# Performance work log

Measured on AMD Instinct MI355X. Metric: run time of the kernel, lower is better.

## Reference

```python
import jax, jax.numpy as jnp
import numpy as np

B, S, HN, TN = 8, 32, 64, 512
HID, EMB, VOCAB = 512, 512, 10000


def setup_inputs():
    key = jax.random.key(0)
    k = jax.random.split(key, 14)
    w = lambda kk, shape: jax.random.normal(kk, shape, jnp.float32) * 0.02
    return {
        "dec_out": jax.random.normal(k[0], (B, S, HID), jnp.float32),
        "history": jax.random.normal(k[1], (B, HID), jnp.float32),
        "head": jax.random.randint(k[2], (B, HN), 0, VOCAB),
        "tail": jax.random.randint(k[3], (B, TN), 0, VOCAB),
        "adj_mask": jax.random.randint(k[4], (B, HN, TN), 0, 2).astype(bool),
        "dup_mask": jax.random.randint(k[5], (B, S, TN), 0, 2).astype(bool),
        "emb_table": w(k[6], (VOCAB, EMB)),
        "W_tq": w(k[7], (2 * HID + EMB, HID)),
        "b_tq": jnp.zeros((HID,), jnp.float32),
        "W_tk": w(k[8], (EMB, HID)),
        "b_tk": jnp.zeros((HID,), jnp.float32),
        "W_tout": w(k[9], (2 * HID, HID)),
        "W_hq": w(k[10], (2 * HID, HID)),
        "b_hq": jnp.zeros((HID,), jnp.float32),
        "W_hk": w(k[11], (HID, HID)),
        "b_hk": jnp.zeros((HID,), jnp.float32),
    }


def reference(dec_out, history, head, tail, adj_mask, dup_mask, emb_table,
              W_tq, b_tq, W_tk, b_tk, W_tout, W_hq, b_hq, W_hk, b_hk):
    head_emb = emb_table[head]  # (B, HN, EMB)
    tail_emb = emb_table[tail]  # (B, TN, EMB)

    # --- tail attention query: Linear(cat([dec_out, history, head_emb])) + ELU.
    # Same math as the torch broadcast-concat, computed as a sum of three
    # partial matmuls to avoid materializing the (B,S,HN,2*hid+emb) concat.
    Wd, Wh, We = W_tq[:HID], W_tq[HID:2 * HID], W_tq[2 * HID:]
    tq = jax.nn.elu((dec_out @ Wd)[:, :, None, :]
                    + (history @ Wh)[:, None, None, :]
                    + (head_emb @ We)[:, None, :, :]
                    + b_tq)                       # (B, S, HN, HID)
    tq = tq.reshape(B, S * HN, HID)
    tk = jax.nn.elu(tail_emb @ W_tk + b_tk)       # (B, TN, HID)  (dropout=eval)

    # combined logical mask: allowed = adjacency AND not-duplicate
    mask = (adj_mask[:, None, :, :] & ~dup_mask[:, :, None, :]).reshape(B, S * HN, TN)

    # GlobalAttention (dot): score -> mask -> softmax -> context -> tanh(linear_out([c;q]))
    scores = jnp.einsum('bqh,bth->bqt', tq, tk)   # (B, S*HN, TN)
    tail_attn = jax.nn.softmax(jnp.where(mask, scores, -jnp.inf), axis=-1)
    ctx = jnp.einsum('bqt,bth->bqh', tail_attn, tk)
    graph_hid = jnp.tanh(ctx @ W_tout[:HID] + tq @ W_tout[HID:])
    graph_hid = graph_hid.reshape(B * S, HN, HID)
    tail_attn = tail_attn.reshape(B * S, HN, TN)

    # --- head attention (one-step), length-masked over HN
    hq = jax.nn.elu(dec_out @ W_hq[:HID] + (history @ W_hq[HID:])[:, None, :] + b_hq)
    hq = hq.reshape(B * S, HID)
    hk = jax.nn.elu(jnp.einsum('nkh,hd->nkd', graph_hid, W_hk) + b_hk)
    lengths = jnp.repeat(jnp.sum(head != 0, axis=-1), S)          # (B*S,)
    hscores = jnp.einsum('nh,nkh->nk', hq, hk)                    # (B*S, HN)
    lmask = jnp.arange(HN)[None, :] < lengths[:, None]
    head_attn = jax.nn.softmax(jnp.where(lmask, hscores, -jnp.inf), axis=-1)
    # (head-attention context output is discarded by the original module)

    prob = jnp.einsum('nk,nkt->nt', head_attn, tail_attn).reshape(B, S, TN)
    return jnp.log(prob + 1e-20)
```

## Files before the change

### kernel.cpp

```cpp
#include <hip/hip_runtime.h>
#include <math.h>

#define BB 8
#define SS 32
#define HN 64
#define TN 512
#define HID 512

typedef __attribute__((ext_vector_type(8))) short short8;
typedef __attribute__((ext_vector_type(4))) float f32x4;

__device__ __forceinline__ float eluf(float x) { return x > 0.f ? x : (expf(x) - 1.f); }

__device__ __forceinline__ short f2bs(float f) {
    union { float f; unsigned int u; } v; v.f = f;
    unsigned int r = v.u + 0x7fffu + ((v.u >> 16) & 1u);
    return (short)(r >> 16);
}
__device__ __forceinline__ float b2f(short s) {
    union { unsigned int u; float f; } v;
    v.u = ((unsigned int)(unsigned short)s) << 16;
    return v.f;
}

__device__ __forceinline__ void gld16(const void* g, void* l) {
    __builtin_amdgcn_global_load_lds(
        (const __attribute__((address_space(1))) void*)g,
        (__attribute__((address_space(3))) void*)l, 16, 0, 0);
}

template <int ACT, int OUTB>
__device__ __forceinline__ void gcore(
    const short* __restrict__ A, const short* __restrict__ B,
    const float* __restrict__ bias, void* __restrict__ Cv,
    int ldc, int K, int m0, int n0, int cm0, short* Ls)
{
    short* Al = Ls;
    short* Bl = Ls + 8192;
    const int tid  = threadIdx.x;
    const int lane = tid & 63;
    const int w    = tid >> 6;
    const int wr   = w >> 1, wc = w & 1;
    const int l16  = lane & 15, quad = lane >> 4;

    const int srow = w * 16 + (lane >> 2);
    const int scol = (lane & 3) * 8;

    f32x4 acc[4][4];
#pragma unroll
    for (int i = 0; i < 4; ++i)
#pragma unroll
        for (int j = 0; j < 4; ++j) { acc[i][j][0]=0.f; acc[i][j][1]=0.f; acc[i][j][2]=0.f; acc[i][j][3]=0.f; }

    short* lA = Al + w * 512;
    short* lB = Bl + w * 512;
    const long rstep = (long)64 * K;

    const short* Ag = A + (long)(m0 + srow) * K + scol;
    const short* Bg = B + (long)(n0 + srow) * K + scol;
    for (int kt = 0; kt < K; kt += 64) {
        __syncthreads();
        gld16(Ag + kt, lA);
        gld16(Ag + kt + rstep, lA + 2048);
        gld16(Ag + kt + 32, lA + 4096);
        gld16(Ag + kt + 32 + rstep, lA + 4096 + 2048);
        gld16(Bg + kt, lB);
        gld16(Bg + kt + rstep, lB + 2048);
        gld16(Bg + kt + 32, lB + 4096);
        gld16(Bg + kt + 32 + rstep, lB + 4096 + 2048);
        __syncthreads();
#pragma unroll
        for (int h = 0; h < 2; ++h) {
            short8 af[4], bf4[4];
#pragma unroll
            for (int mi = 0; mi < 4; ++mi)
                af[mi] = *(const short8*)(Al + h * 4096 + (wr * 64 + mi * 16 + l16) * 32 + quad * 8);
#pragma unroll
            for (int ni = 0; ni < 4; ++ni)
                bf4[ni] = *(const short8*)(Bl + h * 4096 + (wc * 64 + ni * 16 + l16) * 32 + quad * 8);
#pragma unroll
            for (int mi = 0; mi < 4; ++mi)
#pragma unroll
                for (int ni = 0; ni < 4; ++ni)
                    acc[mi][ni] = __builtin_amdgcn_mfma_f32_16x16x32_bf16(af[mi], bf4[ni], acc[mi][ni], 0, 0, 0);
        }
    }

    __syncthreads();

    float bv[4];
#pragma unroll
    for (int ni = 0; ni < 4; ++ni)
        bv[ni] = bias ? bias[n0 + wc * 64 + ni * 16 + l16] : 0.f;

    if (OUTB == 1) {
        short* eb = Ls + w * 1152;
        const int er = lane >> 2;
        const int ec = (lane & 3) * 16;
#pragma unroll
        for (int mi = 0; mi < 4; ++mi) {
#pragma unroll
            for (int ni = 0; ni < 4; ++ni)
#pragma unroll
                for (int r = 0; r < 4; ++r) {
                    float x = acc[mi][ni][r] + bv[ni];
                    if (ACT == 1) x = eluf(x);
                    eb[(quad * 4 + r) * 72 + ni * 16 + l16] = f2bs(x);
                }
            __builtin_amdgcn_sched_barrier(0);
            short8 v0 = *(const short8*)&eb[er * 72 + ec];
            short8 v1 = *(const short8*)&eb[er * 72 + ec + 8];
            long cb = (long)(cm0 + wr * 64 + mi * 16 + er) * ldc + n0 + wc * 64 + ec;
            *(short8*)((short*)Cv + cb)     = v0;
            *(short8*)((short*)Cv + cb + 8) = v1;
            __builtin_amdgcn_sched_barrier(0);
        }
    } else {
#pragma unroll
        for (int mi = 0; mi < 4; ++mi)
#pragma unroll
            for (int ni = 0; ni < 4; ++ni) {
                int gc = n0 + wc * 64 + ni * 16 + l16;
#pragma unroll
                for (int r = 0; r < 4; ++r) {
                    float x = acc[mi][ni][r] + bv[ni];
                    if (ACT == 1) x = eluf(x);
                    ((float*)Cv)[(long)(cm0 + wr * 64 + mi * 16 + quad * 4 + r) * ldc + gc] = x;
                }
            }
    }
}

template <int ACT, int OUTB, int DUAL>
__device__ __forceinline__ void gcoreB(
    const short* __restrict__ A, const short* __restrict__ B,
    const short* __restrict__ A2, const short* __restrict__ B2,
    const float* __restrict__ bias, void* __restrict__ Cv,
    int ldc, int K, int m0, int n0, int cm0, short* Ls,
    const float* __restrict__ hq, float* __restrict__ hsp)
{
    short* Al = Ls;
    short* Bl = Ls + 16384;
    const int tid  = threadIdx.x;
    const int lane = tid & 63;
    const int w    = tid >> 6;
    const int wr   = w >> 1, wc = w & 1;
    const int l16  = lane & 15, quad = lane >> 4;

    const int srow = w * 16 + (lane >> 2);
    const int scol = (lane & 3) * 8;

    f32x4 acc[4][4];
#pragma unroll
    for (int i = 0; i < 4; ++i)
#pragma unroll
        for (int j = 0; j < 4; ++j) { acc[i][j][0]=0.f; acc[i][j][1]=0.f; acc[i][j][2]=0.f; acc[i][j][3]=0.f; }

    short* lA = Al + w * 512;
    short* lB = Bl + w * 512;
    const long rstep = (long)64 * K;

    for (int rep = 0; rep <= DUAL; ++rep) {
        const short* Ag = (rep ? A2 : A) + (long)(m0 + srow) * K + scol;
        const short* Bg = (rep ? B2 : B) + (long)(n0 + srow) * K + scol;
        for (int kt = 0; kt < K; kt += 128) {
            __syncthreads();
#pragma unroll
            for (int h = 0; h < 4; ++h) {
                gld16(Ag + kt + h * 32,         lA + h * 4096);
                gld16(Ag + kt + h * 32 + rstep, lA + h * 4096 + 2048);
                gld16(Bg + kt + h * 32,         lB + h * 4096);
                gld16(Bg + kt + h * 32 + rstep, lB + h * 4096 + 2048);
            }
            __syncthreads();
#pragma unroll
            for (int h = 0; h < 4; ++h) {
                short8 af[4], bf4[4];
#pragma unroll
                for (int mi = 0; mi < 4; ++mi)
                    af[mi] = *(const short8*)(Al + h * 4096 + (wr * 64 + mi * 16 + l16) * 32 + quad * 8);
#pragma unroll
                for (int ni = 0; ni < 4; ++ni)
                    bf4[ni] = *(const short8*)(Bl + h * 4096 + (wc * 64 + ni * 16 + l16) * 32 + quad * 8);
#pragma unroll
                for (int mi = 0; mi < 4; ++mi)
#pragma unroll
                    for (int ni = 0; ni < 4; ++ni)
                        acc[mi][ni] = __builtin_amdgcn_mfma_f32_16x16x32_bf16(af[mi], bf4[ni], acc[mi][ni], 0, 0, 0);
            }
        }
    }

    __syncthreads();

    float bv[4];
#pragma unroll
    for (int ni = 0; ni < 4; ++ni)
        bv[ni] = bias ? bias[n0 + wc * 64 + ni * 16 + l16] : 0.f;

    if (OUTB == 1) {
        short* eb = Ls + w * 1152;
        const int er = lane >> 2;
        const int ec = (lane & 3) * 16;
#pragma unroll
        for (int mi = 0; mi < 4; ++mi) {
#pragma unroll
            for (int ni = 0; ni < 4; ++ni)
#pragma unroll
                for (int r = 0; r < 4; ++r) {
                    float x = acc[mi][ni][r] + bv[ni];
                    if (ACT == 1) x = eluf(x);
                    else if (ACT == 2) x = tanhf(x);
                    eb[(quad * 4 + r) * 72 + ni * 16 + l16] = f2bs(x);
                }
            __builtin_amdgcn_sched_barrier(0);
            short8 v0 = *(const short8*)&eb[er * 72 + ec];
            short8 v1 = *(const short8*)&eb[er * 72 + ec + 8];
            long cb = (long)(cm0 + wr * 64 + mi * 16 + er) * ldc + n0 + wc * 64 + ec;
            *(short8*)((short*)Cv + cb)     = v0;
            *(short8*)((short*)Cv + cb + 8) = v1;
            __builtin_amdgcn_sched_barrier(0);
        }
    } else if (OUTB == 2) {
        const int n_w = (cm0 + wr * 64) >> 6;
        float hqv[4];
#pragma unroll
        for (int ni = 0; ni < 4; ++ni)
            hqv[ni] = hq[(long)n_w * 512 + n0 + wc * 64 + ni * 16 + l16];
        float* red = (float*)Ls;
#pragma unroll
        for (int mi = 0; mi < 4; ++mi)
#pragma unroll
            for (int r = 0; r < 4; ++r) {
                float p = 0.f;
#pragma unroll
                for (int ni = 0; ni < 4; ++ni) {
                    float x = acc[mi][ni][r] + bv[ni];
                    if (ACT == 1) x = eluf(x);
                    p += x * hqv[ni];
                }
                p += __shfl_xor(p, 1);
                p += __shfl_xor(p, 2);
                p += __shfl_xor(p, 4);
                p += __shfl_xor(p, 8);
                if (l16 == 0) red[w * 64 + mi * 16 + quad * 4 + r] = p;
            }
        __syncthreads();
        if (tid < 128) {
            int wr2 = tid >> 6, rw = tid & 63;
            float v = red[(wr2 * 2 + 0) * 64 + rw] + red[(wr2 * 2 + 1) * 64 + rw];
            hsp[(long)(n0 >> 7) * 16384 + cm0 + tid] = v;
        }
    }
}

template <int ACT, int OUTB, int DUAL, int NYL2>
__global__ __launch_bounds__(256) void mgemm_sw(
    const short* __restrict__ A, long sAz,
    const short* __restrict__ B, long sBz,
    const short* __restrict__ A2, long sA2z,
    const short* __restrict__ B2,
    const float* __restrict__ bias,
    void* __restrict__ Cv, long sCz, int ldc, int K)
{
    __shared__ short Ls[32768];
    const int bid = blockIdx.x;
    const int g = (bid & 7) + 8 * (bid >> 5);
    const int x = (bid >> 3) & 3;
    const int y = g & ((1 << NYL2) - 1);
    const int z = g >> NYL2;
    void* C = (void*)((short*)Cv + (long)z * sCz);
    const short* A2z = DUAL ? (A2 + (long)z * sA2z) : nullptr;
    gcoreB<ACT, OUTB, DUAL>(A + (long)z * sAz, B + (long)z * sBz, A2z, B2, bias, C,
                            ldc, K, y * 128, x * 128, y * 128, Ls, nullptr, nullptr);
}

__global__ __launch_bounds__(256) void mgemm_hs(
    const short* __restrict__ A, const short* __restrict__ B,
    const float* __restrict__ bias, const float* __restrict__ hq, float* __restrict__ hsp)
{
    __shared__ short Ls[32768];
    const int bid = blockIdx.x;
    const int y = (bid & 7) + 8 * (bid >> 5);
    const int x = (bid >> 3) & 3;
    gcoreB<1, 2, 0>(A, B, nullptr, nullptr, bias, nullptr, 512, 512,
                    y * 128, x * 128, y * 128, Ls, hq, hsp);
}

__global__ __launch_bounds__(256) void mgemm_multi(
    const short* __restrict__ decb, const short* __restrict__ WTall, float* __restrict__ qall,
    const short* __restrict__ embAll, const short* __restrict__ WTe, float* __restrict__ qe,
    const short* __restrict__ WTk, const float* __restrict__ b_tk, short* __restrict__ tkb)
{
    __shared__ short Ls[16384];
    int id = blockIdx.x;
    if (id < 48) {
        int y = id >> 4, x = id & 15;
        gcore<0, 0>(decb, WTall, nullptr, qall, 2048, 512, y * 128, x * 128, y * 128, Ls);
    } else if (id < 64) {
        int id2 = id - 48, y = id2 >> 2, x = id2 & 3;
        gcore<0, 0>(embAll, WTe, nullptr, qe, 512, 512, y * 128, x * 128, y * 128, Ls);
    } else {
        int id3 = id - 64, y = id3 >> 2, x = id3 & 3;
        gcore<1, 1>(embAll, WTk, b_tk, tkb, 512, 512, 512 + y * 128, x * 128, y * 128, Ls);
    }
}

struct WTDesc { const float* src[9]; short* dst[9]; };

__global__ __launch_bounds__(256) void prep(
    const float* __restrict__ dec_out, const float* __restrict__ history,
    short* __restrict__ decb,
    const float* __restrict__ emb, const int* __restrict__ head, const int* __restrict__ tail,
    short* __restrict__ embAll, WTDesc wd)
{
    __shared__ float t[32][33];
    const int id = blockIdx.x, tid = threadIdx.x;
    if (id < 132) {
        int i = (id * 256 + tid) * 4;
        float4 v = (i < 131072) ? *(const float4*)(dec_out + i)
                                : *(const float4*)(history + (i - 131072));
        short4 o;
        o.x = f2bs(v.x); o.y = f2bs(v.y); o.z = f2bs(v.z); o.w = f2bs(v.w);
        *(short4*)(decb + i) = o;
    } else if (id < 132 + 2304) {
        int r = (id - 132) * 2 + (tid >> 7);
        int c4 = (tid & 127) * 4;
        int idx = (r < 512) ? head[r] : tail[r - 512];
        float4 v = *(const float4*)(emb + (long)idx * 512 + c4);
        short4 o;
        o.x = f2bs(v.x); o.y = f2bs(v.y); o.z = f2bs(v.z); o.w = f2bs(v.w);
        *(short4*)(embAll + (long)r * 512 + c4) = o;
    } else {
        int q = id - 2436;
        int z = q >> 8, xy = q & 255;
        int x = xy & 15, y = xy >> 4;
        const float* src = wd.src[z];
        short* dst = wd.dst[z];
        int k0 = y * 32, n0 = x * 32;
        int tx = tid & 31, ty = tid >> 5;
#pragma unroll
        for (int i = 0; i < 32; i += 8)
            t[ty + i][tx] = src[(long)(k0 + ty + i) * 512 + n0 + tx];
        __syncthreads();
#pragma unroll
        for (int i = 0; i < 32; i += 8)
            dst[(long)(n0 + ty + i) * 512 + k0 + tx] = f2bs(t[tx][ty + i]);
    }
}

__global__ __launch_bounds__(256) void l3_kernel(
    const float* __restrict__ qall, const float* __restrict__ qe,
    const float* __restrict__ b_tq, short* __restrict__ tqb,
    const short* __restrict__ WTo1, const short* __restrict__ tkb, short* __restrict__ tkWTb,
    const float* __restrict__ b_hq, float* __restrict__ hqf)
{
    __shared__ short Ls[16384];
    if (blockIdx.x < 8192) {
        long gid = (long)blockIdx.x * 256 + threadIdx.x;
        int r = (int)(gid >> 7), j0 = ((int)gid & 127) * 4;
        int b = r >> 11, rem = r & 2047, s = rem >> 6, h = rem & 63;
        float4 d = *(const float4*)(qall + (long)(b * 32 + s) * 2048 + j0);
        float4 q = *(const float4*)(qall + (long)(256 + b) * 2048 + 1024 + j0);
        float4 e = *(const float4*)(qe + (long)(b * 64 + h) * 512 + j0);
        float4 bb = *(const float4*)(b_tq + j0);
        short4 o;
        o.x = f2bs(eluf(d.x + q.x + e.x + bb.x));
        o.y = f2bs(eluf(d.y + q.y + e.y + bb.y));
        o.z = f2bs(eluf(d.z + q.z + e.z + bb.z));
        o.w = f2bs(eluf(d.w + q.w + e.w + bb.w));
        *(short4*)(tqb + (long)r * 512 + j0) = o;
    } else if (blockIdx.x < 8320) {
        int id2 = blockIdx.x - 8192;
        int z = id2 >> 4, r = id2 & 15;
        int x = r & 3, y = r >> 2;
        gcore<0, 1>(WTo1, tkb + (long)z * 262144, nullptr,
                    tkWTb + (long)z * 262144, 512, 512, y * 128, x * 128, y * 128, Ls);
    } else {
        long gid = (long)(blockIdx.x - 8320) * 256 + threadIdx.x;
        int n = (int)(gid >> 7), j0 = ((int)gid & 127) * 4;
        int b = n >> 5;
        float4 d = *(const float4*)(qall + (long)n * 2048 + 512 + j0);
        float4 h2 = *(const float4*)(qall + (long)(256 + b) * 2048 + 1536 + j0);
        float4 bb = *(const float4*)(b_hq + j0);
        float4 o;
        o.x = eluf(d.x + h2.x + bb.x);
        o.y = eluf(d.y + h2.y + bb.y);
        o.z = eluf(d.z + h2.z + bb.z);
        o.w = eluf(d.w + h2.w + bb.w);
        *(float4*)(hqf + (long)n * 512 + j0) = o;
    }
}

__global__ __launch_bounds__(256) void sm_kernel(
    const short* __restrict__ sc, const int* __restrict__ adj, const int* __restrict__ dup,
    short* __restrict__ Pb)
{
    int w = threadIdx.x >> 6, lane = threadIdx.x & 63;
    long r = (long)blockIdx.x * 4 + w;
    int b = (int)(r >> 11), rem = (int)(r & 2047), s = rem >> 6, h = rem & 63;
    const short* row = sc + r * 512 + lane * 8;
    const int* adjr = adj + ((long)(b * 64 + h)) * 512 + lane * 8;
    const int* dupr = dup + ((long)(b * 32 + s)) * 512 + lane * 8;
    short8 v8 = *(const short8*)row;
    int4 a0 = *(const int4*)adjr, a1 = *(const int4*)(adjr + 4);
    int4 d0 = *(const int4*)dupr, d1 = *(const int4*)(dupr + 4);
    int am[8] = {a0.x, a0.y, a0.z, a0.w, a1.x, a1.y, a1.z, a1.w};
    int dm[8] = {d0.x, d0.y, d0.z, d0.w, d1.x, d1.y, d1.z, d1.w};
    float v[8];
    float m = -INFINITY;
#pragma unroll
    for (int i = 0; i < 8; ++i) {
        v[i] = (am[i] && !dm[i]) ? b2f(v8[i]) : -INFINITY;
        m = fmaxf(m, v[i]);
    }
#pragma unroll
    for (int d = 32; d >= 1; d >>= 1) m = fmaxf(m, __shfl_xor(m, d));
    float sum = 0.f;
#pragma unroll
    for (int i = 0; i < 8; ++i) {
        float e = (m == -INFINITY) ? 0.f : expf(v[i] - m);
        v[i] = e; sum += e;
    }
#pragma unroll
    for (int d = 32; d >= 1; d >>= 1) sum += __shfl_xor(sum, d);
    float inv = sum > 0.f ? 1.f / sum : 0.f;
    short8 o;
#pragma unroll
    for (int i = 0; i < 8; ++i) o[i] = f2bs(v[i] * inv);
    *(short8*)(Pb + r * 512 + lane * 8) = o;
}

__global__ __launch_bounds__(256) void fused_head(
    const float* __restrict__ hsp, const int* __restrict__ head,
    const short* __restrict__ ta, float* __restrict__ out)
{
    int n = blockIdx.x, b = n >> 5;
    int tid = threadIdx.x;
    __shared__ float hal[64];
    __shared__ float part[4][512];

    if (tid < 64) {
        float sv_raw = hsp[n * 64 + tid] + hsp[16384 + n * 64 + tid]
                     + hsp[2 * 16384 + n * 64 + tid] + hsp[3 * 16384 + n * 64 + tid];
        int hv = head[b * 64 + tid];
        unsigned long long ball = __ballot(hv != 0);
        int len = __popcll(ball);
        float sv = (tid < len) ? sv_raw : -INFINITY;
        float m = sv;
#pragma unroll
        for (int d = 32; d >= 1; d >>= 1) m = fmaxf(m, __shfl_xor(m, d));
        float e = expf(sv - m);
        float sum = e;
#pragma unroll
        for (int d = 32; d >= 1; d >>= 1) sum += __shfl_xor(sum, d);
        hal[tid] = e / sum;
    }
    __syncthreads();

    {
        int w = tid >> 6, lane = tid & 63;
        const short* tab = ta + (long)n * 64 * 512 + (long)(w * 16) * 512 + lane * 8;
        float acc[8] = {};
#pragma unroll
        for (int k = 0; k < 16; ++k) {
            float a = hal[w * 16 + k];
            short8 tv = *(const short8*)(tab + (long)k * 512);
#pragma unroll
            for (int u = 0; u < 8; ++u) acc[u] += a * b2f(tv[u]);
        }
        float4* pp = (float4*)&part[w][lane * 8];
        pp[0] = make_float4(acc[0], acc[1], acc[2], acc[3]);
        pp[1] = make_float4(acc[4], acc[5], acc[6], acc[7]);
    }
    __syncthreads();

    for (int t = tid; t < 512; t += 256) {
        float a = part[0][t] + part[1][t] + part[2][t] + part[3][t];
        out[(long)n * 512 + t] = logf(a + 1e-20f);
    }
}

extern "C" void kernel_launch(void* const* d_in, const int* in_sizes, int n_in,
                              void* d_out, int out_size, void* d_ws, size_t ws_size,
                              hipStream_t stream)
{
    const float* dec_out = (const float*)d_in[0];
    const float* history = (const float*)d_in[1];
    const int*   head    = (const int*)d_in[2];
    const int*   tail    = (const int*)d_in[3];
    const int*   adj     = (const int*)d_in[4];
    const int*   dup     = (const int*)d_in[5];
    const float* emb     = (const float*)d_in[6];
    const float* W_tq    = (const float*)d_in[7];
    const float* b_tq    = (const float*)d_in[8];
    const float* W_tk    = (const float*)d_in[9];
    const float* b_tk    = (const float*)d_in[10];
    const float* W_tout  = (const float*)d_in[11];
    const float* W_hq    = (const float*)d_in[12];
    const float* b_hq    = (const float*)d_in[13];
    const float* W_hk    = (const float*)d_in[14];
    const float* b_hk    = (const float*)d_in[15];
    float* out = (float*)d_out;

    char* ws = (char*)d_ws;
    auto alloc = [&](size_t bytes) -> void* {
        char* p = ws;
        ws += (bytes + 255) & ~(size_t)255;
        return (void*)p;
    };
    short* decb   = (short*)alloc((size_t)384 * 512 * 2);
    short* embAll = (short*)alloc((size_t)4608 * 512 * 2);
    short* WT     = (short*)alloc((size_t)9 * 512 * 512 * 2);
    float* qall   = (float*)alloc((size_t)384 * 2048 * 4);
    float* qe     = (float*)alloc((size_t)512 * 512 * 4);
    float* hqf    = (float*)alloc((size_t)256 * 512 * 4);
    float* hsp    = (float*)alloc((size_t)4 * 16384 * 4);
    short* tkb    = (short*)alloc((size_t)4096 * 512 * 2);
    short* tkWTb  = (short*)alloc((size_t)4096 * 512 * 2);
    short* tqb    = (short*)alloc((size_t)16384 * 512 * 2);
    short* scb    = (short*)alloc((size_t)16384 * 512 * 2);
    short* Pb     = (short*)alloc((size_t)16384 * 512 * 2);
    short* ghb = scb;

    WTDesc wd;
    wd.src[0] = W_tq;               wd.dst[0] = WT;
    wd.src[1] = W_hq;               wd.dst[1] = WT + (size_t)1 * 262144;
    wd.src[2] = W_tq + 512 * 512;   wd.dst[2] = WT + (size_t)2 * 262144;
    wd.src[3] = W_hq + 512 * 512;   wd.dst[3] = WT + (size_t)3 * 262144;
    wd.src[4] = W_tq + 1024 * 512;  wd.dst[4] = WT + (size_t)4 * 262144;
    wd.src[5] = W_tk;               wd.dst[5] = WT + (size_t)5 * 262144;
    wd.src[6] = W_tout;             wd.dst[6] = WT + (size_t)6 * 262144;
    wd.src[7] = W_tout + 512 * 512; wd.dst[7] = WT + (size_t)7 * 262144;
    wd.src[8] = W_hk;               wd.dst[8] = WT + (size_t)8 * 262144;

    prep<<<4740, 256, 0, stream>>>(dec_out, history, decb, emb, head, tail, embAll, wd);
    mgemm_multi<<<192, 256, 0, stream>>>(decb, WT, qall, embAll, WT + (size_t)4 * 262144, qe,
                                         WT + (size_t)5 * 262144, b_tk, tkb);
    l3_kernel<<<8448, 256, 0, stream>>>(qall, qe, b_tq, tqb, WT + (size_t)6 * 262144, tkb, tkWTb,
                                        b_hq, hqf);
    mgemm_sw<0, 1, 0, 4><<<512, 256, 0, stream>>>(
        tqb, (long)2048 * 512, tkb, 262144, nullptr, 0, nullptr, nullptr,
        scb, (long)2048 * 512, 512, 512);
    sm_kernel<<<4096, 256, 0, stream>>>(scb, adj, dup, Pb);
    mgemm_sw<2, 1, 1, 4><<<512, 256, 0, stream>>>(
        Pb, (long)2048 * 512, tkWTb, 262144, tqb, (long)2048 * 512, WT + (size_t)7 * 262144,
        nullptr, ghb, (long)2048 * 512, 512, 512);
    mgemm_hs<<<512, 256, 0, stream>>>(ghb, WT + (size_t)8 * 262144, b_hk, hqf, hsp);
    fused_head<<<256, 256, 0, stream>>>(hsp, head, Pb, out);
}
```

Baseline: 211.3 us.

## Fuse tail-attention GEMMs, softmax and head attention into one per-(b,s) kernel

Replaces five launches (score GEMM, masked softmax, dual context/output GEMM, head-key GEMM with score reduction, and head softmax plus mixing) with a single kernel of 256 blocks of 512 threads. Each block owns one (b,s) pair, i.e. 64 query rows, and runs all four 64x512x512 GEMMs back to back with a small 32-wide K-step. The softmax, head-attention scoring and final log-mix happen in the same block, so the hsp scratch buffer and the extra launches go away. In exchange there is one block per CU with no load/compute pipelining, and each block re-streams the full 512x512 B matrices from cache for every GEMM. That raises L2 traffic and lowers parallelism compared with the previous 128x128-tiled kernels.

```diff
diff --git a/kernel.cpp b/kernel.cpp
--- a/kernel.cpp
+++ b/kernel.cpp
@@ -131,24 +131,100 @@
     }
 }
 
-template <int ACT, int OUTB, int DUAL>
-__device__ __forceinline__ void gcoreB(
-    const short* __restrict__ A, const short* __restrict__ B,
-    const short* __restrict__ A2, const short* __restrict__ B2,
-    const float* __restrict__ bias, void* __restrict__ Cv,
-    int ldc, int K, int m0, int n0, int cm0, short* Ls,
-    const float* __restrict__ hq, float* __restrict__ hsp)
-{
-    short* Al = Ls;
-    short* Bl = Ls + 16384;
+__device__ __forceinline__ void tgemm512(
+    const short* __restrict__ Arows, const short* __restrict__ B,
+    short* Ls, f32x4 (&acc)[4][4])
+{
     const int tid  = threadIdx.x;
     const int lane = tid & 63;
     const int w    = tid >> 6;
-    const int wr   = w >> 1, wc = w & 1;
     const int l16  = lane & 15, quad = lane >> 4;
-
-    const int srow = w * 16 + (lane >> 2);
-    const int scol = (lane & 3) * 8;
+    short* Al = Ls;
+    short* Bl = Ls + 2048;
+
+    for (int kt = 0; kt < 512; kt += 32) {
+        __syncthreads();
+        if (tid < 256)
+            gld16(Arows + (long)(tid >> 2) * 512 + kt + (tid & 3) * 8, Al + w * 512);
+#pragma unroll
+        for (int j = 0; j < 4; ++j) {
+            int lin = j * 512 + tid;
+            gld16(B + (long)(lin >> 2) * 512 + kt + (lin & 3) * 8, Bl + j * 4096 + w * 512);
+        }
+        __syncthreads();
+        short8 af[4], bf[4];
+#pragma unroll
+        for (int mi = 0; mi < 4; ++mi)
+            af[mi] = *(const short8*)(Al + (mi * 16 + l16) * 32 + quad * 8);
+#pragma unroll
+        for (int ni = 0; ni < 4; ++ni)
+            bf[ni] = *(const short8*)(Bl + (w * 64 + ni * 16 + l16) * 32 + quad * 8);
+#pragma unroll
+        for (int mi = 0; mi < 4; ++mi)
+#pragma unroll
+            for (int ni = 0; ni < 4; ++ni)
+                acc[mi][ni] = __builtin_amdgcn_mfma_f32_16x16x32_bf16(af[mi], bf[ni], acc[mi][ni], 0, 0, 0);
+    }
+}
+
+template <int ACT>
+__device__ __forceinline__ void epi64(
+    f32x4 (&acc)[4][4], short* Ls, short* __restrict__ Crows)
+{
+    const int tid  = threadIdx.x;
+    const int lane = tid & 63;
+    const int w    = tid >> 6;
+    const int l16  = lane & 15, quad = lane >> 4;
+    short* eb = Ls + w * 1152;
+    const int er = lane >> 2;
+    const int ec = (lane & 3) * 16;
+#pragma unroll
+    for (int mi = 0; mi < 4; ++mi) {
+#pragma unroll
+        for (int ni = 0; ni < 4; ++ni)
+#pragma unroll
+            for (int r = 0; r < 4; ++r) {
+                float x = acc[mi][ni][r];
+                if (ACT == 2) x = tanhf(x);
+                eb[(quad * 4 + r) * 72 + ni * 16 + l16] = f2bs(x);
+            }
+        __builtin_amdgcn_sched_barrier(0);
+        short8 v0 = *(const short8*)&eb[er * 72 + ec];
+        short8 v1 = *(const short8*)&eb[er * 72 + ec + 8];
+        long cb = (long)(mi * 16 + er) * 512 + w * 64 + ec;
+        *(short8*)(Crows + cb)     = v0;
+        *(short8*)(Crows + cb + 8) = v1;
+        __builtin_amdgcn_sched_barrier(0);
+    }
+}
+
+__global__ __launch_bounds__(512, 1) void tail_kernel(
+    const short* __restrict__ tqb, const short* __restrict__ tkb,
+    const short* __restrict__ tkWTb, const short* __restrict__ WT,
+    const int* __restrict__ adj, const int* __restrict__ dup,
+    const int* __restrict__ head, const float* __restrict__ b_hk,
+    const float* __restrict__ hqf,
+    short* __restrict__ scb, short* __restrict__ Pb,
+    float* __restrict__ out)
+{
+    __shared__ short Ls[20480];
+    const int tid  = threadIdx.x;
+    const int lane = tid & 63;
+    const int w    = tid >> 6;
+    const int l16  = lane & 15, quad = lane >> 4;
+
+    const int n  = blockIdx.x;
+    const int b  = n >> 5;
+    const int s  = n & 31;
+    const long rb = (long)n * 64;
+
+    const short* tqrows = tqb + rb * 512;
+    const short* tkb_b  = tkb + (long)b * 262144;
+    const short* tkWT_b = tkWTb + (long)b * 262144;
+    const short* WT7    = WT + (size_t)7 * 262144;
+    const short* WT8    = WT + (size_t)8 * 262144;
+    short* scrows = scb + rb * 512;
+    short* Prows  = Pb  + rb * 512;
 
     f32x4 acc[4][4];
 #pragma unroll
@@ -156,153 +232,129 @@
 #pragma unroll
         for (int j = 0; j < 4; ++j) { acc[i][j][0]=0.f; acc[i][j][1]=0.f; acc[i][j][2]=0.f; acc[i][j][3]=0.f; }
 
-    short* lA = Al + w * 512;
-    short* lB = Bl + w * 512;
-    const long rstep = (long)64 * K;
-
-    for (int rep = 0; rep <= DUAL; ++rep) {
-        const short* Ag = (rep ? A2 : A) + (long)(m0 + srow) * K + scol;
-        const short* Bg = (rep ? B2 : B) + (long)(n0 + srow) * K + scol;
-        for (int kt = 0; kt < K; kt += 128) {
-            __syncthreads();
-#pragma unroll
-            for (int h = 0; h < 4; ++h) {
-                gld16(Ag + kt + h * 32,         lA + h * 4096);
-                gld16(Ag + kt + h * 32 + rstep, lA + h * 4096 + 2048);
-                gld16(Bg + kt + h * 32,         lB + h * 4096);
-                gld16(Bg + kt + h * 32 + rstep, lB + h * 4096 + 2048);
-            }
-            __syncthreads();
-#pragma unroll
-            for (int h = 0; h < 4; ++h) {
-                short8 af[4], bf4[4];
-#pragma unroll
-                for (int mi = 0; mi < 4; ++mi)
-                    af[mi] = *(const short8*)(Al + h * 4096 + (wr * 64 + mi * 16 + l16) * 32 + quad * 8);
-#pragma unroll
-                for (int ni = 0; ni < 4; ++ni)
-                    bf4[ni] = *(const short8*)(Bl + h * 4096 + (wc * 64 + ni * 16 + l16) * 32 + quad * 8);
-#pragma unroll
-                for (int mi = 0; mi < 4; ++mi)
-#pragma unroll
-                    for (int ni = 0; ni < 4; ++ni)
-                        acc[mi][ni] = __builtin_amdgcn_mfma_f32_16x16x32_bf16(af[mi], bf4[ni], acc[mi][ni], 0, 0, 0);
-            }
-        }
-    }
-
-    __syncthreads();
-
-    float bv[4];
-#pragma unroll
-    for (int ni = 0; ni < 4; ++ni)
-        bv[ni] = bias ? bias[n0 + wc * 64 + ni * 16 + l16] : 0.f;
-
-    if (OUTB == 1) {
-        short* eb = Ls + w * 1152;
-        const int er = lane >> 2;
-        const int ec = (lane & 3) * 16;
-#pragma unroll
-        for (int mi = 0; mi < 4; ++mi) {
-#pragma unroll
-            for (int ni = 0; ni < 4; ++ni)
-#pragma unroll
-                for (int r = 0; r < 4; ++r) {
-                    float x = acc[mi][ni][r] + bv[ni];
-                    if (ACT == 1) x = eluf(x);
-                    else if (ACT == 2) x = tanhf(x);
-                    eb[(quad * 4 + r) * 72 + ni * 16 + l16] = f2bs(x);
-                }
-            __builtin_amdgcn_sched_barrier(0);
-            short8 v0 = *(const short8*)&eb[er * 72 + ec];
-            short8 v1 = *(const short8*)&eb[er * 72 + ec + 8];
-            long cb = (long)(cm0 + wr * 64 + mi * 16 + er) * ldc + n0 + wc * 64 + ec;
-            *(short8*)((short*)Cv + cb)     = v0;
-            *(short8*)((short*)Cv + cb + 8) = v1;
-            __builtin_amdgcn_sched_barrier(0);
-        }
-    } else if (OUTB == 2) {
-        const int n_w = (cm0 + wr * 64) >> 6;
-        float hqv[4];
-#pragma unroll
-        for (int ni = 0; ni < 4; ++ni)
-            hqv[ni] = hq[(long)n_w * 512 + n0 + wc * 64 + ni * 16 + l16];
-        float* red = (float*)Ls;
+    tgemm512(tqrows, tkb_b, Ls, acc);
+    __syncthreads();
+    epi64<0>(acc, Ls, scrows);
+    __syncthreads();
+
+    for (int j = 0; j < 8; ++j) {
+        int row = w * 8 + j;
+        const short* srow = scrows + (long)row * 512 + lane * 8;
+        const int* adjr = adj + ((long)(b * 64 + row)) * 512 + lane * 8;
+        const int* dupr = dup + ((long)(b * 32 + s)) * 512 + lane * 8;
+        short8 v8 = *(const short8*)srow;
+        int4 a0 = *(const int4*)adjr, a1 = *(const int4*)(adjr + 4);
+        int4 d0 = *(const int4*)dupr, d1 = *(const int4*)(dupr + 4);
+        int am[8] = {a0.x, a0.y, a0.z, a0.w, a1.x, a1.y, a1.z, a1.w};
+        int dm[8] = {d0.x, d0.y, d0.z, d0.w, d1.x, d1.y, d1.z, d1.w};
+        float v[8];
+        float m = -INFINITY;
+#pragma unroll
+        for (int i = 0; i < 8; ++i) {
+            v[i] = (am[i] && !dm[i]) ? b2f(v8[i]) : -INFINITY;
+            m = fmaxf(m, v[i]);
+        }
+#pragma unroll
+        for (int d = 32; d >= 1; d >>= 1) m = fmaxf(m, __shfl_xor(m, d));
+        float sum = 0.f;
+#pragma unroll
+        for (int i = 0; i < 8; ++i) {
+            float e = (m == -INFINITY) ? 0.f : expf(v[i] - m);
+            v[i] = e; sum += e;
+        }
+#pragma unroll
+        for (int d = 32; d >= 1; d >>= 1) sum += __shfl_xor(sum, d);
+        float inv = sum > 0.f ? 1.f / sum : 0.f;
+        short8 o;
+#pragma unroll
+        for (int i = 0; i < 8; ++i) o[i] = f2bs(v[i] * inv);
+        *(short8*)(Prows + (long)row * 512 + lane * 8) = o;
+    }
+
+#pragma unroll
+    for (int i = 0; i < 4; ++i)
+#pragma unroll
+        for (int j = 0; j < 4; ++j) { acc[i][j][0]=0.f; acc[i][j][1]=0.f; acc[i][j][2]=0.f; acc[i][j][3]=0.f; }
+    tgemm512(Prows, tkWT_b, Ls, acc);
+    tgemm512(tqrows, WT7, Ls, acc);
+    __syncthreads();
+    epi64<2>(acc, Ls, scrows);
+
+#pragma unroll
+    for (int i = 0; i < 4; ++i)
+#pragma unroll
+        for (int j = 0; j < 4; ++j) { acc[i][j][0]=0.f; acc[i][j][1]=0.f; acc[i][j][2]=0.f; acc[i][j][3]=0.f; }
+    tgemm512(scrows, WT8, Ls, acc);
+    __syncthreads();
+
+    float* redf  = (float*)Ls;
+    float* hal   = (float*)Ls + 512;
+    float* partf = (float*)Ls + 576;
+    {
+        float bv[4], hqv[4];
+#pragma unroll
+        for (int ni = 0; ni < 4; ++ni) {
+            int col = w * 64 + ni * 16 + l16;
+            bv[ni]  = b_hk[col];
+            hqv[ni] = hqf[(long)n * 512 + col];
+        }
 #pragma unroll
         for (int mi = 0; mi < 4; ++mi)
 #pragma unroll
             for (int r = 0; r < 4; ++r) {
                 float p = 0.f;
 #pragma unroll
-                for (int ni = 0; ni < 4; ++ni) {
-                    float x = acc[mi][ni][r] + bv[ni];
-                    if (ACT == 1) x = eluf(x);
-                    p += x * hqv[ni];
-                }
+                for (int ni = 0; ni < 4; ++ni)
+                    p += eluf(acc[mi][ni][r] + bv[ni]) * hqv[ni];
                 p += __shfl_xor(p, 1);
                 p += __shfl_xor(p, 2);
                 p += __shfl_xor(p, 4);
                 p += __shfl_xor(p, 8);
-                if (l16 == 0) red[w * 64 + mi * 16 + quad * 4 + r] = p;
+                if (l16 == 0) redf[w * 64 + mi * 16 + quad * 4 + r] = p;
             }
-        __syncthreads();
-        if (tid < 128) {
-            int wr2 = tid >> 6, rw = tid & 63;
-            float v = red[(wr2 * 2 + 0) * 64 + rw] + red[(wr2 * 2 + 1) * 64 + rw];
-            hsp[(long)(n0 >> 7) * 16384 + cm0 + tid] = v;
-        }
-    }
-}
-
-template <int ACT, int OUTB, int DUAL, int NYL2>
-__global__ __launch_bounds__(256) void mgemm_sw(
-    const short* __restrict__ A, long sAz,
-    const short* __restrict__ B, long sBz,
-    const short* __restrict__ A2, long sA2z,
-    const short* __restrict__ B2,
-    const float* __restrict__ bias,
-    void* __restrict__ Cv, long sCz, int ldc, int K)
-{
-    __shared__ short Ls[32768];
-    const int bid = blockIdx.x;
-    const int g = (bid & 7) + 8 * (bid >> 5);
-    const int x = (bid >> 3) & 3;
-    const int y = g & ((1 << NYL2) - 1);
-    const int z = g >> NYL2;
-    void* C = (void*)((short*)Cv + (long)z * sCz);
-    const short* A2z = DUAL ? (A2 + (long)z * sA2z) : nullptr;
-    gcoreB<ACT, OUTB, DUAL>(A + (long)z * sAz, B + (long)z * sBz, A2z, B2, bias, C,
-                            ldc, K, y * 128, x * 128, y * 128, Ls, nullptr, nullptr);
-}
-
-__global__ __launch_bounds__(256) void mgemm_hs(
-    const short* __restrict__ A, const short* __restrict__ B,
-    const float* __restrict__ bias, const float* __restrict__ hq, float* __restrict__ hsp)
-{
-    __shared__ short Ls[32768];
-    const int bid = blockIdx.x;
-    const int y = (bid & 7) + 8 * (bid >> 5);
-    const int x = (bid >> 3) & 3;
-    gcoreB<1, 2, 0>(A, B, nullptr, nullptr, bias, nullptr, 512, 512,
-                    y * 128, x * 128, y * 128, Ls, hq, hsp);
-}
-
-__global__ __launch_bounds__(256) void mgemm_multi(
-    const short* __restrict__ decb, const short* __restrict__ WTall, float* __restrict__ qall,
-    const short* __restrict__ embAll, const short* __restrict__ WTe, float* __restrict__ qe,
-    const short* __restrict__ WTk, const float* __restrict__ b_tk, short* __restrict__ tkb)
-{
-    __shared__ short Ls[16384];
-    int id = blockIdx.x;
-    if (id < 48) {
-        int y = id >> 4, x = id & 15;
-        gcore<0, 0>(decb, WTall, nullptr, qall, 2048, 512, y * 128, x * 128, y * 128, Ls);
-    } else if (id < 64) {
-        int id2 = id - 48, y = id2 >> 2, x = id2 & 3;
-        gcore<0, 0>(embAll, WTe, nullptr, qe, 512, 512, y * 128, x * 128, y * 128, Ls);
-    } else {
-        int id3 = id - 64, y = id3 >> 2, x = id3 & 3;
-        gcore<1, 1>(embAll, WTk, b_tk, tkb, 512, 512, 512 + y * 128, x * 128, y * 128, Ls);
+    }
+    __syncthreads();
+
+    if (tid < 64) {
+        float sv_raw = 0.f;
+#pragma unroll
+        for (int w2 = 0; w2 < 8; ++w2) sv_raw += redf[w2 * 64 + tid];
+        int hv = head[b * 64 + tid];
+        unsigned long long ball = __ballot(hv != 0);
+        int len = __popcll(ball);
+        float sv = (tid < len) ? sv_raw : -INFINITY;
+        float m = sv;
+#pragma unroll
+        for (int d = 32; d >= 1; d >>= 1) m = fmaxf(m, __shfl_xor(m, d));
+        float e = expf(sv - m);
+        float sum = e;
+#pragma unroll
+        for (int d = 32; d >= 1; d >>= 1) sum += __shfl_xor(sum, d);
+        hal[tid] = e / sum;
+    }
+    __syncthreads();
+
+    {
+        const short* tab = Prows + (long)(w * 8) * 512 + lane * 8;
+        float a2[8] = {};
+#pragma unroll
+        for (int k = 0; k < 8; ++k) {
+            float a = hal[w * 8 + k];
+            short8 tv = *(const short8*)(tab + (long)k * 512);
+#pragma unroll
+            for (int u = 0; u < 8; ++u) a2[u] += a * b2f(tv[u]);
+        }
+        float4* pp = (float4*)&partf[w * 512 + lane * 8];
+        pp[0] = make_float4(a2[0], a2[1], a2[2], a2[3]);
+        pp[1] = make_float4(a2[4], a2[5], a2[6], a2[7]);
+    }
+    __syncthreads();
+
+    {
+        float a = 0.f;
+#pragma unroll
+        for (int w2 = 0; w2 < 8; ++w2) a += partf[w2 * 512 + tid];
+        out[(long)n * 512 + tid] = logf(a + 1e-20f);
     }
 }
 
@@ -346,6 +398,25 @@
 #pragma unroll
         for (int i = 0; i < 32; i += 8)
             dst[(long)(n0 + ty + i) * 512 + k0 + tx] = f2bs(t[tx][ty + i]);
+    }
+}
+
+__global__ __launch_bounds__(256) void mgemm_multi(
+    const short* __restrict__ decb, const short* __restrict__ WTall, float* __restrict__ qall,
+    const short* __restrict__ embAll, const short* __restrict__ WTe, float* __restrict__ qe,
+    const short* __restrict__ WTk, const float* __restrict__ b_tk, short* __restrict__ tkb)
+{
+    __shared__ short Ls[16384];
+    int id = blockIdx.x;
+    if (id < 48) {
+        int y = id >> 4, x = id & 15;
+        gcore<0, 0>(decb, WTall, nullptr, qall, 2048, 512, y * 128, x * 128, y * 128, Ls);
+    } else if (id < 64) {
+        int id2 = id - 48, y = id2 >> 2, x = id2 & 3;
+        gcore<0, 0>(embAll, WTe, nullptr, qe, 512, 512, y * 128, x * 128, y * 128, Ls);
+    } else {
+        int id3 = id - 64, y = id3 >> 2, x = id3 & 3;
+        gcore<1, 1>(embAll, WTk, b_tk, tkb, 512, 512, 512 + y * 128, x * 128, y * 128, Ls);
     }
 }
 
@@ -392,95 +463,6 @@
     }
 }
 
-__global__ __launch_bounds__(256) void sm_kernel(
-    const short* __restrict__ sc, const int* __restrict__ adj, const int* __restrict__ dup,
-    short* __restrict__ Pb)
-{
-    int w = threadIdx.x >> 6, lane = threadIdx.x & 63;
-    long r = (long)blockIdx.x * 4 + w;
-    int b = (int)(r >> 11), rem = (int)(r & 2047), s = rem >> 6, h = rem & 63;
-    const short* row = sc + r * 512 + lane * 8;
-    const int* adjr = adj + ((long)(b * 64 + h)) * 512 + lane * 8;
-    const int* dupr = dup + ((long)(b * 32 + s)) * 512 + lane * 8;
-    short8 v8 = *(const short8*)row;
-    int4 a0 = *(const int4*)adjr, a1 = *(const int4*)(adjr + 4);
-    int4 d0 = *(const int4*)dupr, d1 = *(const int4*)(dupr + 4);
-    int am[8] = {a0.x, a0.y, a0.z, a0.w, a1.x, a1.y, a1.z, a1.w};
-    int dm[8] = {d0.x, d0.y, d0.z, d0.w, d1.x, d1.y, d1.z, d1.w};
-    float v[8];
-    float m = -INFINITY;
-#pragma unroll
-    for (int i = 0; i < 8; ++i) {
-        v[i] = (am[i] && !dm[i]) ? b2f(v8[i]) : -INFINITY;
-        m = fmaxf(m, v[i]);
-    }
-#pragma unroll
-    for (int d = 32; d >= 1; d >>= 1) m = fmaxf(m, __shfl_xor(m, d));
-    float sum = 0.f;
-#pragma unroll
-    for (int i = 0; i < 8; ++i) {
-        float e = (m == -INFINITY) ? 0.f : expf(v[i] - m);
-        v[i] = e; sum += e;
-    }
-#pragma unroll
-    for (int d = 32; d >= 1; d >>= 1) sum += __shfl_xor(sum, d);
-    float inv = sum > 0.f ? 1.f / sum : 0.f;
-    short8 o;
-#pragma unroll
-    for (int i = 0; i < 8; ++i) o[i] = f2bs(v[i] * inv);
-    *(short8*)(Pb + r * 512 + lane * 8) = o;
-}
-
-__global__ __launch_bounds__(256) void fused_head(
-    const float* __restrict__ hsp, const int* __restrict__ head,
-    const short* __restrict__ ta, float* __restrict__ out)
-{
-    int n = blockIdx.x, b = n >> 5;
-    int tid = threadIdx.x;
-    __shared__ float hal[64];
-    __shared__ float part[4][512];
-
-    if (tid < 64) {
-        float sv_raw = hsp[n * 64 + tid] + hsp[16384 + n * 64 + tid]
-                     + hsp[2 * 16384 + n * 64 + tid] + hsp[3 * 16384 + n * 64 + tid];
-        int hv = head[b * 64 + tid];
-        unsigned long long ball = __ballot(hv != 0);
-        int len = __popcll(ball);
-        float sv = (tid < len) ? sv_raw : -INFINITY;
-        float m = sv;
-#pragma unroll
-        for (int d = 32; d >= 1; d >>= 1) m = fmaxf(m, __shfl_xor(m, d));
-        float e = expf(sv - m);
-        float sum = e;
-#pragma unroll
-        for (int d = 32; d >= 1; d >>= 1) sum += __shfl_xor(sum, d);
-        hal[tid] = e / sum;
-    }
-    __syncthreads();
-
-    {
-        int w = tid >> 6, lane = tid & 63;
-        const short* tab = ta + (long)n * 64 * 512 + (long)(w * 16) * 512 + lane * 8;
-        float acc[8] = {};
-#pragma unroll
-        for (int k = 0; k < 16; ++k) {
-            float a = hal[w * 16 + k];
-            short8 tv = *(const short8*)(tab + (long)k * 512);
-#pragma unroll
-            for (int u = 0; u < 8; ++u) acc[u] += a * b2f(tv[u]);
-        }
-        float4* pp = (float4*)&part[w][lane * 8];
-        pp[0] = make_float4(acc[0], acc[1], acc[2], acc[3]);
-        pp[1] = make_float4(acc[4], acc[5], acc[6], acc[7]);
-    }
-    __syncthreads();
-
-    for (int t = tid; t < 512; t += 256) {
-        float a = part[0][t] + part[1][t] + part[2][t] + part[3][t];
-        out[(long)n * 512 + t] = logf(a + 1e-20f);
-    }
-}
-
 extern "C" void kernel_launch(void* const* d_in, const int* in_sizes, int n_in,
                               void* d_out, int out_size, void* d_ws, size_t ws_size,
                               hipStream_t stream)
@@ -515,13 +497,11 @@
     float* qall   = (float*)alloc((size_t)384 * 2048 * 4);
     float* qe     = (float*)alloc((size_t)512 * 512 * 4);
     float* hqf    = (float*)alloc((size_t)256 * 512 * 4);
-    float* hsp    = (float*)alloc((size_t)4 * 16384 * 4);
     short* tkb    = (short*)alloc((size_t)4096 * 512 * 2);
     short* tkWTb  = (short*)alloc((size_t)4096 * 512 * 2);
     short* tqb    = (short*)alloc((size_t)16384 * 512 * 2);
     short* scb    = (short*)alloc((size_t)16384 * 512 * 2);
     short* Pb     = (short*)alloc((size_t)16384 * 512 * 2);
-    short* ghb = scb;
 
     WTDesc wd;
     wd.src[0] = W_tq;               wd.dst[0] = WT;
@@ -539,13 +519,6 @@
                                          WT + (size_t)5 * 262144, b_tk, tkb);
     l3_kernel<<<8448, 256, 0, stream>>>(qall, qe, b_tq, tqb, WT + (size_t)6 * 262144, tkb, tkWTb,
                                         b_hq, hqf);
-    mgemm_sw<0, 1, 0, 4><<<512, 256, 0, stream>>>(
-        tqb, (long)2048 * 512, tkb, 262144, nullptr, 0, nullptr, nullptr,
-        scb, (long)2048 * 512, 512, 512);
-    sm_kernel<<<4096, 256, 0, stream>>>(scb, adj, dup, Pb);
-    mgemm_sw<2, 1, 1, 4><<<512, 256, 0, stream>>>(
-        Pb, (long)2048 * 512, tkWTb, 262144, tqb, (long)2048 * 512, WT + (size_t)7 * 262144,
-        nullptr, ghb, (long)2048 * 512, 512, 512);
-    mgemm_hs<<<512, 256, 0, stream>>>(ghb, WT + (size_t)8 * 262144, b_hk, hqf, hsp);
-    fused_head<<<256, 256, 0, stream>>>(hsp, head, Pb, out);
-}
+    tail_kernel<<<256, 512, 0, stream>>>(tqb, tkb, tkWTb, WT, adj, dup, head, b_hk, hqf,
+                                         scb, Pb, out);
+}
```

Result: slower. 230.2 us (+9.0%).
